# Optimization experiments

Hardware: AMD Instinct MI355X
Metric: run time of the kernel (lower is better)

## Reference

```python
import jax, jax.numpy as jnp
import numpy as np

E, IN, OUT, T = 8, 2048, 5632, 16384
_GROUP_SIZES = np.array([1024, 3072, 512, 4096, 2048, 1536, 2560, 1536])  # sums to T


def setup_inputs() -> dict:
    key = jax.random.key(0)
    k1, k2 = jax.random.split(key)
    x = jax.random.normal(k1, (T, IN), dtype=jnp.float32)
    # Expert weights [num_experts, out_features, in_features], kaiming-ish scale
    weight = jax.random.normal(k2, (E, OUT, IN), dtype=jnp.float32) * (1.0 / np.sqrt(IN))
    offsets = jnp.asarray(np.concatenate([[0], np.cumsum(_GROUP_SIZES)]), dtype=jnp.int32)
    return {"input": x, "weight": weight, "expert_offsets": offsets}


def reference(input, weight, expert_offsets):
    """Grouped GEMM: output[s_i:e_i] = input[s_i:e_i] @ weight[i].T (bias=None).

    Tokens are pre-sorted by expert; expert_offsets [E+1] gives each expert's
    contiguous token range. Offsets are routing metadata (static w.r.t. math),
    so we read them as concrete ints and loop over the small fixed expert set.
    """
    offs = np.asarray(jax.device_get(expert_offsets))
    num_experts = weight.shape[0]
    outs = []
    for i in range(num_experts):
        s, e = int(offs[i]), int(offs[i + 1])
        # [m_i, in] @ [in, out] -> [m_i, out]
        outs.append(input[s:e] @ weight[i].T)
    return jnp.concatenate(outs, axis=0)  # [total_tokens, out_features]
```

## Files before the change

kernel.cpp:

```cpp
#include <hip/hip_runtime.h>
#include <hip/hip_bf16.h>


#define T_TOK 16384
#define K_IN  2048
#define N_OUT 5632
#define NEXP  8

typedef __attribute__((ext_vector_type(8))) short short8;
typedef __attribute__((ext_vector_type(4))) float f32x4;
typedef unsigned short ushort_t;

__device__ __forceinline__ ushort_t f2bf(float x) {
  __hip_bfloat16 h = __float2bfloat16(x);
  return *reinterpret_cast<ushort_t*>(&h);
}

__global__ void __launch_bounds__(256) cvt2(const float* __restrict__ x,
                                            const float* __restrict__ w,
                                            ushort_t* __restrict__ ox,
                                            ushort_t* __restrict__ ow,
                                            int n8x, int n8t) {
  int i = blockIdx.x * blockDim.x + threadIdx.x;
  int stride = gridDim.x * blockDim.x;
  for (; i < n8t; i += stride) {
    const float* src;
    ushort_t* dst;
    int j;
    if (i < n8x) { src = x; dst = ox; j = i; }
    else         { src = w; dst = ow; j = i - n8x; }
    const float4* p = (const float4*)src + (size_t)j * 2;
    float4 a = p[0], b = p[1];
    short8 v;
    v[0] = (short)f2bf(a.x); v[1] = (short)f2bf(a.y);
    v[2] = (short)f2bf(a.z); v[3] = (short)f2bf(a.w);
    v[4] = (short)f2bf(b.x); v[5] = (short)f2bf(b.y);
    v[6] = (short)f2bf(b.z); v[7] = (short)f2bf(b.w);
    *((short8*)dst + j) = v;
  }
}

#define MT2 64
#define NT2 22
#define GRID2 (MT2 * NT2)

#define BAR() do { asm volatile("" ::: "memory"); \
                   __builtin_amdgcn_s_barrier(); \
                   asm volatile("" ::: "memory"); } while (0)
#define VMCNT(n) asm volatile("s_waitcnt vmcnt(" #n ")" ::: "memory")
#define LDF(p, imm) (*(const short8*)((p) + (imm)))

template <int M0>
__device__ __forceinline__ void mma_pair(f32x4 acc[8][4], const short8 a0[2],
                                         const short8 a1[2],
                                         const short8 bF[4][2]) {
  __builtin_amdgcn_s_setprio(1);
#pragma unroll
  for (int n = 0; n < 4; ++n)
#pragma unroll
    for (int s = 0; s < 2; ++s) {
      acc[M0][n] = __builtin_amdgcn_mfma_f32_16x16x32_bf16(a0[s], bF[n][s],
                                                           acc[M0][n], 0, 0, 0);
      acc[M0 + 1][n] = __builtin_amdgcn_mfma_f32_16x16x32_bf16(
          a1[s], bF[n][s], acc[M0 + 1][n], 0, 0, 0);
    }
  __builtin_amdgcn_s_setprio(0);
}

__global__ void __launch_bounds__(512, 2) gemm8(
    const ushort_t* __restrict__ abf, const ushort_t* __restrict__ wbf,
    const int* __restrict__ offs, float* __restrict__ out) {
  __shared__ __align__(16) ushort_t lds[2][2][2][8192];

  int bid = blockIdx.x;
  int wg = (bid & 7) * (GRID2 / 8) + (bid >> 3);
  int tm = wg / NT2;
  int tn = wg - tm * NT2;

  const int t = threadIdx.x;
  const int w = t >> 6;
  const int l = t & 63;
  const int wm = w >> 2;
  const int wn = w & 3;

  const int row0 = tm * 256;
  int e = 0;
#pragma unroll
  for (int i = 1; i < NEXP; ++i) e += (row0 >= offs[i]) ? 1 : 0;

  const ushort_t* aB = abf + (size_t)row0 * K_IN;
  const ushort_t* wB =
      wbf + (size_t)e * N_OUT * K_IN + (size_t)(tn * 256) * K_IN;
  const size_t H = (size_t)128 * K_IN;

  const size_t srow = (size_t)(2 * w) * 8 + (l >> 3);
  const int scol = ((l & 7) ^ (l >> 3)) * 8;
  const ushort_t* const sA0 = aB + srow * K_IN + scol;
  const ushort_t* const sA1 = aB + (srow + 8) * K_IN + scol;
  const ushort_t* const sW0 = wB + srow * K_IN + scol;
  const ushort_t* const sW1 = wB + (srow + 8) * K_IN + scol;

  auto stage2 = [&](const ushort_t* s0, const ushort_t* s1, ushort_t* lreg,
                    size_t ko) {
    __builtin_amdgcn_global_load_lds(
        (const __attribute__((address_space(1))) void*)(s0 + ko),
        (__attribute__((address_space(3))) void*)(lreg + (2 * w) * 512), 16, 0, 0);
    __builtin_amdgcn_global_load_lds(
        (const __attribute__((address_space(1))) void*)(s1 + ko),
        (__attribute__((address_space(3))) void*)(lreg + (2 * w + 1) * 512), 16, 0, 0);
  };

  f32x4 acc[8][4];
#pragma unroll
  for (int i = 0; i < 8; ++i)
#pragma unroll
    for (int j = 0; j < 4; ++j)
#pragma unroll
      for (int r = 0; r < 4; ++r) acc[i][j][r] = 0.f;

  const int l15 = l & 15;
  const int kgo2 = (l >> 4) * 16;
  const int swz = (l15 & 7) << 4;
  const int fo0 = l15 * 128 + (kgo2 ^ swz);
  const int fo1 = l15 * 128 + ((64 + kgo2) ^ swz);
  const char* aP[2][2];
  const char* bP[2][2];
#pragma unroll
  for (int b = 0; b < 2; ++b) {
    aP[b][0] = (const char*)&lds[b][0][wm][0] + fo0;
    aP[b][1] = (const char*)&lds[b][0][wm][0] + fo1;
    bP[b][0] = (const char*)&lds[b][1][wn >> 1][0] + (wn & 1) * 8192 + fo0;
    bP[b][1] = (const char*)&lds[b][1][wn >> 1][0] + (wn & 1) * 8192 + fo1;
  }

#define LDA_PAIR(d0, d1, buf, m)                          \
  do {                                                    \
    d0[0] = LDF(aP[buf][0], (m) * 2048);                  \
    d0[1] = LDF(aP[buf][1], (m) * 2048);                  \
    d1[0] = LDF(aP[buf][0], ((m) + 1) * 2048);            \
    d1[1] = LDF(aP[buf][1], ((m) + 1) * 2048);            \
  } while (0)
#define LDB_ALL(dst, buf)                                 \
  do {                                                    \
    _Pragma("unroll")                                     \
    for (int n = 0; n < 4; ++n) {                         \
      dst[n][0] = LDF(bP[buf][0], n * 2048);              \
      dst[n][1] = LDF(bP[buf][1], n * 2048);              \
    }                                                     \
  } while (0)

  stage2(sA0, sA1, &lds[0][0][0][0], 0);
  stage2(sA0, sA1, &lds[0][0][1][0], H);
  stage2(sW0, sW1, &lds[0][1][0][0], 0);
  stage2(sW0, sW1, &lds[0][1][1][0], H);
  stage2(sW0, sW1, &lds[1][1][0][0], 64);
  stage2(sW0, sW1, &lds[1][1][1][0], H + 64);
  VMCNT(4);
  BAR();

  short8 bF[4][2];
  short8 r0a[2], r0b[2];
  short8 r1a[2], r1b[2];

  LDB_ALL(bF, 0);
  LDA_PAIR(r0a, r0b, 0, 0);

#pragma unroll 1
  for (int J = 0; J < 16; ++J) {
    const size_t kO1 = (size_t)(2 * J + 1) * 64;
    const size_t kO2 = (size_t)(2 * J + 2) * 64;
    const size_t kO3 = (size_t)(2 * J + 3) * 64;
    const bool more = (J < 15);

    LDA_PAIR(r1a, r1b, 0, 2);
    stage2(sA0, sA1, &lds[1][0][0][0], kO1);
    BAR(); mma_pair<0>(acc, r0a, r0b, bF); BAR();

    LDA_PAIR(r0a, r0b, 0, 4);
    stage2(sA0, sA1, &lds[1][0][1][0], H + kO1);
    BAR(); mma_pair<2>(acc, r1a, r1b, bF); BAR();

    LDA_PAIR(r1a, r1b, 0, 6);
    if (more) stage2(sW0, sW1, &lds[0][1][0][0], kO2);
    BAR(); mma_pair<4>(acc, r0a, r0b, bF); BAR();

    if (more) stage2(sW0, sW1, &lds[0][1][1][0], H + kO2);
    BAR(); mma_pair<6>(acc, r1a, r1b, bF);
    if (more) { VMCNT(4); } else { VMCNT(0); }
    LDB_ALL(bF, 1);
    LDA_PAIR(r0a, r0b, 1, 0);
    BAR();

    LDA_PAIR(r1a, r1b, 1, 2);
    if (more) stage2(sA0, sA1, &lds[0][0][0][0], kO2);
    BAR(); mma_pair<0>(acc, r0a, r0b, bF); BAR();

    LDA_PAIR(r0a, r0b, 1, 4);
    if (more) stage2(sA0, sA1, &lds[0][0][1][0], H + kO2);
    BAR(); mma_pair<2>(acc, r1a, r1b, bF); BAR();

    LDA_PAIR(r1a, r1b, 1, 6);
    if (more) stage2(sW0, sW1, &lds[1][1][0][0], kO3);
    BAR(); mma_pair<4>(acc, r0a, r0b, bF); BAR();

    if (more) stage2(sW0, sW1, &lds[1][1][1][0], H + kO3);
    BAR(); mma_pair<6>(acc, r1a, r1b, bF);
    if (more) {
      VMCNT(4);
      LDB_ALL(bF, 0);
      LDA_PAIR(r0a, r0b, 0, 0);
    }
    BAR();
  }

  const int cr = (l >> 4) * 4;
  const int cc = l & 15;
  float* ob = out + (size_t)(row0 + wm * 128) * N_OUT + tn * 256 + wn * 64;
#pragma unroll
  for (int m = 0; m < 8; ++m)
#pragma unroll
    for (int n = 0; n < 4; ++n)
#pragma unroll
      for (int r = 0; r < 4; ++r)
        ob[(size_t)(m * 16 + cr + r) * N_OUT + n * 16 + cc] = acc[m][n][r];
#undef LDA_PAIR
#undef LDB_ALL
}

#define BM 128
#define BN 128
#define BK 64
#define MT (T_TOK / BM)
#define NTILE (N_OUT / BN)

__global__ void __launch_bounds__(256) gemm_fb(const float* __restrict__ af,
                                               const float* __restrict__ wf,
                                               const int* __restrict__ offs,
                                               float* __restrict__ out) {
  __shared__ __align__(16) ushort_t lsA[BM * BK];
  __shared__ __align__(16) ushort_t lsB[BN * BK];
  int bid = blockIdx.x;
  int wg = (bid & 7) * ((MT * NTILE) >> 3) + (bid >> 3);
  int tm = wg / NTILE, tn = wg - tm * NTILE;
  const int t = threadIdx.x, w = t >> 6, l = t & 63;
  const int row0 = tm * BM;
  int e = 0;
#pragma unroll
  for (int i = 1; i < NEXP; ++i) e += (row0 >= offs[i]) ? 1 : 0;
  const size_t wbase = (size_t)e * ((size_t)N_OUT * K_IN);
  f32x4 acc[4][4];
#pragma unroll
  for (int i = 0; i < 4; ++i)
#pragma unroll
    for (int j = 0; j < 4; ++j)
#pragma unroll
      for (int r = 0; r < 4; ++r) acc[i][j][r] = 0.f;
  const int wm = w >> 1, wn = w & 1;
  const int rA = wm * 64 + (l & 15), rB = wn * 64 + (l & 15);
  const int kgo = (l >> 4) * 8;
  for (int kt = 0; kt < K_IN / BK; ++kt) {
    const int k0 = kt * BK;
    if (kt) __syncthreads();
#pragma unroll
    for (int p = 0; p < 4; ++p) {
      const int ia = (p * 4 + w) * 64 + l;
      const float4* g = (const float4*)(af + (size_t)(row0 + (ia >> 3)) * K_IN +
                                        k0 + (ia & 7) * 8);
      float4 a = g[0], b = g[1];
      short8 v;
      v[0] = (short)f2bf(a.x); v[1] = (short)f2bf(a.y);
      v[2] = (short)f2bf(a.z); v[3] = (short)f2bf(a.w);
      v[4] = (short)f2bf(b.x); v[5] = (short)f2bf(b.y);
      v[6] = (short)f2bf(b.z); v[7] = (short)f2bf(b.w);
      *(short8*)&lsA[ia * 8] = v;
    }
#pragma unroll
    for (int p = 0; p < 4; ++p) {
      const int ib = (p * 4 + w) * 64 + l;
      const float4* g = (const float4*)(wf + wbase +
                                        (size_t)(tn * BN + (ib >> 3)) * K_IN +
                                        k0 + (ib & 7) * 8);
      float4 a = g[0], b = g[1];
      short8 v;
      v[0] = (short)f2bf(a.x); v[1] = (short)f2bf(a.y);
      v[2] = (short)f2bf(a.z); v[3] = (short)f2bf(a.w);
      v[4] = (short)f2bf(b.x); v[5] = (short)f2bf(b.y);
      v[6] = (short)f2bf(b.z); v[7] = (short)f2bf(b.w);
      *(short8*)&lsB[ib * 8] = v;
    }
    __syncthreads();
#pragma unroll
    for (int s = 0; s < 2; ++s) {
      const int ko = s * 32 + kgo;
      short8 aF[4], bFf[4];
#pragma unroll
      for (int i = 0; i < 4; ++i) aF[i] = *(const short8*)&lsA[(rA + i * 16) * BK + ko];
#pragma unroll
      for (int j = 0; j < 4; ++j) bFf[j] = *(const short8*)&lsB[(rB + j * 16) * BK + ko];
#pragma unroll
      for (int i = 0; i < 4; ++i)
#pragma unroll
        for (int j = 0; j < 4; ++j)
          acc[i][j] = __builtin_amdgcn_mfma_f32_16x16x32_bf16(aF[i], bFf[j],
                                                              acc[i][j], 0, 0, 0);
    }
  }
  const int cr = (l >> 4) * 4, cc = l & 15;
  float* ob = out + (size_t)(row0 + wm * 64) * N_OUT + tn * BN + wn * 64;
#pragma unroll
  for (int i = 0; i < 4; ++i)
#pragma unroll
    for (int j = 0; j < 4; ++j)
#pragma unroll
      for (int r = 0; r < 4; ++r)
        ob[(size_t)(i * 16 + cr + r) * N_OUT + j * 16 + cc] = acc[i][j][r];
}

extern "C" void kernel_launch(void* const* d_in, const int* in_sizes, int n_in,
                              void* d_out, int out_size, void* d_ws, size_t ws_size,
                              hipStream_t stream) {
  const float* x = (const float*)d_in[0];
  const float* wt = (const float*)d_in[1];
  const int* offs = (const int*)d_in[2];
  float* out = (float*)d_out;

  const size_t nA = (size_t)T_TOK * K_IN;
  const size_t nW = (size_t)NEXP * N_OUT * K_IN;
  const size_t need = (nA + nW) * sizeof(ushort_t);

  if (ws_size >= need) {
    ushort_t* abf = (ushort_t*)d_ws;
    ushort_t* wbf = abf + nA;
    cvt2<<<2048, 256, 0, stream>>>(x, wt, abf, wbf, (int)(nA / 8),
                                   (int)((nA + nW) / 8));
    gemm8<<<GRID2, 512, 0, stream>>>(abf, wbf, offs, out);
  } else {
    gemm_fb<<<MT * NTILE, 256, 0, stream>>>(x, wt, offs, out);
  }
}
```

Measured before the change: 514.3 us.

## Interleave MFMA with LDS and global loads via sched_group_barrier and peel last iteration

Restructures the main K loop of the grouped GEMM kernel. It removes one barrier per phase so each MFMA block overlaps the global-to-LDS staging and the LDS fragment reads for the next phase. Explicit sched_group_barrier hints interleave MFMA, DS-read and VMEM instructions. The first A-stage and fragment loads are hoisted into the prologue, and the final iteration is peeled so the `more` branches disappear. Dropping barriers risks LDS read/write hazards if a buffer is overwritten while other waves still read it, and changes how much prefetch is in flight.

New measurement: 501.9 us. 1.02x faster.

```diff
diff --git a/kernel.cpp b/kernel.cpp
--- a/kernel.cpp
+++ b/kernel.cpp
@@ -50,6 +50,27 @@
 #define VMCNT(n) asm volatile("s_waitcnt vmcnt(" #n ")" ::: "memory")
 #define LDF(p, imm) (*(const short8*)((p) + (imm)))
 
+__device__ __forceinline__ void sgb_x() {
+  __builtin_amdgcn_sched_group_barrier(0x010, 2, 0);
+#pragma unroll
+  for (int i = 0; i < 4; ++i) {
+    __builtin_amdgcn_sched_group_barrier(0x008, 4, 0);
+    __builtin_amdgcn_sched_group_barrier(0x100, 1, 0);
+  }
+}
+__device__ __forceinline__ void sgb_y() {
+  __builtin_amdgcn_sched_group_barrier(0x010, 2, 0);
+  __builtin_amdgcn_sched_group_barrier(0x008, 16, 0);
+}
+__device__ __forceinline__ void sgb_z() {
+  __builtin_amdgcn_sched_group_barrier(0x010, 2, 0);
+#pragma unroll
+  for (int i = 0; i < 8; ++i) {
+    __builtin_amdgcn_sched_group_barrier(0x008, 2, 0);
+    __builtin_amdgcn_sched_group_barrier(0x100, 2, 0);
+  }
+}
+
 template <int M0>
 __device__ __forceinline__ void mma_pair(f32x4 acc[8][4], const short8 a0[2],
                                          const short8 a1[2],
@@ -155,62 +176,101 @@
   stage2(sW0, sW1, &lds[0][1][1][0], H);
   stage2(sW0, sW1, &lds[1][1][0][0], 64);
   stage2(sW0, sW1, &lds[1][1][1][0], H + 64);
-  VMCNT(4);
+  stage2(sA0, sA1, &lds[1][0][0][0], 64);
+  VMCNT(6);
   BAR();
 
   short8 bF[4][2];
   short8 r0a[2], r0b[2];
   short8 r1a[2], r1b[2];
-
   LDB_ALL(bF, 0);
   LDA_PAIR(r0a, r0b, 0, 0);
+  LDA_PAIR(r1a, r1b, 0, 2);
 
 #pragma unroll 1
-  for (int J = 0; J < 16; ++J) {
+  for (int J = 0; J < 15; ++J) {
     const size_t kO1 = (size_t)(2 * J + 1) * 64;
     const size_t kO2 = (size_t)(2 * J + 2) * 64;
     const size_t kO3 = (size_t)(2 * J + 3) * 64;
-    const bool more = (J < 15);
-
-    LDA_PAIR(r1a, r1b, 0, 2);
-    stage2(sA0, sA1, &lds[1][0][0][0], kO1);
-    BAR(); mma_pair<0>(acc, r0a, r0b, bF); BAR();
-
+
+    sgb_x();
+    mma_pair<0>(acc, r0a, r0b, bF);
+    stage2(sA0, sA1, &lds[1][0][1][0], H + kO1);
     LDA_PAIR(r0a, r0b, 0, 4);
-    stage2(sA0, sA1, &lds[1][0][1][0], H + kO1);
-    BAR(); mma_pair<2>(acc, r1a, r1b, bF); BAR();
-
+    BAR();
+    sgb_x();
+    mma_pair<2>(acc, r1a, r1b, bF);
+    stage2(sW0, sW1, &lds[0][1][0][0], kO2);
     LDA_PAIR(r1a, r1b, 0, 6);
-    if (more) stage2(sW0, sW1, &lds[0][1][0][0], kO2);
-    BAR(); mma_pair<4>(acc, r0a, r0b, bF); BAR();
-
-    if (more) stage2(sW0, sW1, &lds[0][1][1][0], H + kO2);
-    BAR(); mma_pair<6>(acc, r1a, r1b, bF);
-    if (more) { VMCNT(4); } else { VMCNT(0); }
+    BAR();
+    sgb_y();
+    mma_pair<4>(acc, r0a, r0b, bF);
+    stage2(sW0, sW1, &lds[0][1][1][0], H + kO2);
+    VMCNT(4);
+    BAR();
+    sgb_z();
+    mma_pair<6>(acc, r1a, r1b, bF);
     LDB_ALL(bF, 1);
     LDA_PAIR(r0a, r0b, 1, 0);
-    BAR();
-
+    stage2(sA0, sA1, &lds[0][0][0][0], kO2);
     LDA_PAIR(r1a, r1b, 1, 2);
-    if (more) stage2(sA0, sA1, &lds[0][0][0][0], kO2);
-    BAR(); mma_pair<0>(acc, r0a, r0b, bF); BAR();
-
+    BAR();
+    sgb_x();
+    mma_pair<0>(acc, r0a, r0b, bF);
+    stage2(sA0, sA1, &lds[0][0][1][0], H + kO2);
     LDA_PAIR(r0a, r0b, 1, 4);
-    if (more) stage2(sA0, sA1, &lds[0][0][1][0], H + kO2);
-    BAR(); mma_pair<2>(acc, r1a, r1b, bF); BAR();
-
+    BAR();
+    sgb_x();
+    mma_pair<2>(acc, r1a, r1b, bF);
+    stage2(sW0, sW1, &lds[1][1][0][0], kO3);
     LDA_PAIR(r1a, r1b, 1, 6);
-    if (more) stage2(sW0, sW1, &lds[1][1][0][0], kO3);
-    BAR(); mma_pair<4>(acc, r0a, r0b, bF); BAR();
-
-    if (more) stage2(sW0, sW1, &lds[1][1][1][0], H + kO3);
-    BAR(); mma_pair<6>(acc, r1a, r1b, bF);
-    if (more) {
-      VMCNT(4);
-      LDB_ALL(bF, 0);
-      LDA_PAIR(r0a, r0b, 0, 0);
-    }
-    BAR();
+    BAR();
+    sgb_y();
+    mma_pair<4>(acc, r0a, r0b, bF);
+    stage2(sW0, sW1, &lds[1][1][1][0], H + kO3);
+    VMCNT(4);
+    BAR();
+    sgb_z();
+    mma_pair<6>(acc, r1a, r1b, bF);
+    LDB_ALL(bF, 0);
+    LDA_PAIR(r0a, r0b, 0, 0);
+    stage2(sA0, sA1, &lds[1][0][0][0], kO3);
+    LDA_PAIR(r1a, r1b, 0, 2);
+    BAR();
+  }
+
+  {
+    sgb_x();
+    mma_pair<0>(acc, r0a, r0b, bF);
+    stage2(sA0, sA1, &lds[1][0][1][0], H + 1984);
+    LDA_PAIR(r0a, r0b, 0, 4);
+    BAR();
+    sgb_x();
+    mma_pair<2>(acc, r1a, r1b, bF);
+    LDA_PAIR(r1a, r1b, 0, 6);
+    BAR();
+    sgb_y();
+    mma_pair<4>(acc, r0a, r0b, bF);
+    VMCNT(0);
+    BAR();
+    sgb_z();
+    mma_pair<6>(acc, r1a, r1b, bF);
+    LDB_ALL(bF, 1);
+    LDA_PAIR(r0a, r0b, 1, 0);
+    LDA_PAIR(r1a, r1b, 1, 2);
+    BAR();
+    sgb_x();
+    mma_pair<0>(acc, r0a, r0b, bF);
+    LDA_PAIR(r0a, r0b, 1, 4);
+    BAR();
+    sgb_x();
+    mma_pair<2>(acc, r1a, r1b, bF);
+    LDA_PAIR(r1a, r1b, 1, 6);
+    BAR();
+    sgb_y();
+    mma_pair<4>(acc, r0a, r0b, bF);
+    BAR();
+    mma_pair<6>(acc, r1a, r1b, bF);
   }
 
   const int cr = (l >> 4) * 4;
```
